# Kernel optimization log

Measured on AMD Instinct MI355X. Metric: run time of the kernel, lower is better.

The kernel has to match this reference:

```python
import jax, jax.numpy as jnp
import numpy as np


def setup_inputs() -> dict:
    key = jax.random.key(0)
    kx, ky, kw = jax.random.split(key, 3)
    B, N, M = 8, 4096, 4096
    x = jax.random.normal(kx, (B, N, 3), dtype=jnp.float32)
    y = jax.random.normal(ky, (B, M, 3), dtype=jnp.float32)
    weight = jax.random.uniform(kw, (B,), dtype=jnp.float32)
    return {"x": x, "y": y, "weight": weight}


def reference(x, y, weight):
    # (mathematically identical to sum((x-y)^2), avoids the (B,N,M,3) tensor)
    x2 = jnp.sum(x * x, axis=-1)                     # (B, N)
    y2 = jnp.sum(y * y, axis=-1)                     # (B, M)
    xy = jnp.einsum('bnd,bmd->bnm', x, y)            # (B, N, M)
    dist = jnp.maximum(x2[:, :, None] + y2[:, None, :] - 2.0 * xy, 0.0)
    dist_x_min = jnp.min(dist, axis=2)               # (B, N) nearest-in-y per x
    dist_y_min = jnp.min(dist, axis=1)               # (B, M) nearest-in-x per y
    # point_reduction='mean', bidirectional=True
    loss = jnp.mean(dist_x_min, axis=1) + jnp.mean(dist_y_min, axis=1)  # (B,)
    loss = loss * weight
    # batch_reduction='mean'
    return jnp.mean(loss)
```

## Files before the change

kernel.cpp:

```cpp
#include <hip/hip_runtime.h>
#include <math.h>


constexpr int BATCH = 8;
constexpr int NP    = 4096;
constexpr int T     = 1024;
constexpr int QPB   = 256;
constexpr int KPT   = 8;
constexpr int S     = 32;
constexpr int TPS   = 128;

__global__ __launch_bounds__(T, 4) void chamfer_main(
    const float* __restrict__ x, const float* __restrict__ y,
    const float* __restrict__ w, float* __restrict__ ps)
{
    const int bid = blockIdx.x;
    const int dir = bid >> 7;
    const int b   = (bid >> 4) & 7;
    const int qc  = bid & 15;

    const float* q = dir ? y : x;
    const float* t = dir ? x : y;

    __shared__ float4 ty[NP];
    __shared__ float  pmin[S / 2][QPB];
    __shared__ float  qn[QPB];
    __shared__ float  rsum[T / 64];

    const int tid = threadIdx.x;

    const float* tb = t + (size_t)b * NP * 3;
    for (int j = tid; j < NP; j += T) {
        float t0 = tb[3 * j + 0];
        float t1 = tb[3 * j + 1];
        float t2 = tb[3 * j + 2];
        ty[j] = make_float4(t0, t1, t2, fmaf(t0, t0, fmaf(t1, t1, t2 * t2)));
    }

    const int qrow  = tid & 31;
    const int slice = tid >> 5;
    const int n0 = b * NP + qc * QPB + qrow * KPT;
    const float4* qb = reinterpret_cast<const float4*>(q + (size_t)n0 * 3);
    float4 v0 = qb[0], v1 = qb[1], v2 = qb[2], v3 = qb[3], v4 = qb[4], v5 = qb[5];
    float px[KPT][3] = {
        {v0.x, v0.y, v0.z}, {v0.w, v1.x, v1.y},
        {v1.z, v1.w, v2.x}, {v2.y, v2.z, v2.w},
        {v3.x, v3.y, v3.z}, {v3.w, v4.x, v4.y},
        {v4.z, v4.w, v5.x}, {v5.y, v5.z, v5.w},
    };
    float xn[KPT][3], mn[KPT];
    #pragma unroll
    for (int k = 0; k < KPT; ++k) {
        float x2 = fmaf(px[k][0], px[k][0],
                   fmaf(px[k][1], px[k][1], px[k][2] * px[k][2]));
        if (slice == 0) qn[qrow * KPT + k] = x2;
        #pragma unroll
        for (int d = 0; d < 3; ++d) xn[k][d] = -2.0f * px[k][d];
        mn[k] = INFINITY;
    }

    __syncthreads();

    const int j0 = slice * TPS;
    #pragma unroll 4
    for (int j = j0; j < j0 + TPS; j += 2) {
        float4 ta = ty[j];
        float4 tc = ty[j + 1];
        #pragma unroll
        for (int k = 0; k < KPT; ++k) {
            float da = fmaf(xn[k][0], ta.x,
                       fmaf(xn[k][1], ta.y, fmaf(xn[k][2], ta.z, ta.w)));
            float db = fmaf(xn[k][0], tc.x,
                       fmaf(xn[k][1], tc.y, fmaf(xn[k][2], tc.z, tc.w)));
            float m;
            asm("v_min3_f32 %0, %1, %2, %3"
                : "=v"(m) : "v"(mn[k]), "v"(da), "v"(db));
            mn[k] = m;
        }
    }

    #pragma unroll
    for (int k = 0; k < KPT; ++k)
        mn[k] = fminf(mn[k], __shfl_xor(mn[k], 32, 64));
    if ((slice & 1) == 0) {
        #pragma unroll
        for (int k = 0; k < KPT; ++k)
            pmin[slice >> 1][qrow * KPT + k] = mn[k];
    }
    __syncthreads();

    float val = 0.0f;
    if (tid < QPB) {
        float m = pmin[0][tid];
        #pragma unroll
        for (int s = 1; s < S / 2; ++s) m = fminf(m, pmin[s][tid]);
        val = fmaxf(qn[tid] + m, 0.0f);
    }

    for (int off = 32; off; off >>= 1) val += __shfl_down(val, off, 64);
    if ((tid & 63) == 0) rsum[tid >> 6] = val;
    __syncthreads();
    if (tid == 0) {
        float s = 0.0f;
        #pragma unroll
        for (int i = 0; i < T / 64; ++i) s += rsum[i];
        ps[bid] = s * w[b] * (1.0f / ((float)NP * (float)BATCH));
    }
}

__global__ __launch_bounds__(256) void chamfer_final(
    const float* __restrict__ ps, float* __restrict__ out)
{
    const int tid = threadIdx.x;
    float v = ps[tid];
    for (int off = 32; off; off >>= 1) v += __shfl_down(v, off, 64);
    __shared__ float red[4];
    if ((tid & 63) == 0) red[tid >> 6] = v;
    __syncthreads();
    if (tid == 0) out[0] = (red[0] + red[1]) + (red[2] + red[3]);
}

extern "C" void kernel_launch(void* const* d_in, const int* in_sizes, int n_in,
                              void* d_out, int out_size, void* d_ws, size_t ws_size,
                              hipStream_t stream) {
    const float* x = (const float*)d_in[0];
    const float* y = (const float*)d_in[1];
    const float* w = (const float*)d_in[2];
    float* out = (float*)d_out;
    float* ps  = (float*)d_ws;

    chamfer_main<<<256, T, 0, stream>>>(x, y, w, ps);
    chamfer_final<<<1, 256, 0, stream>>>(ps, out);
}
```

Before: 26.91 us.

## Raise queries per thread to sixteen and shrink final reduction to one wavefront

Each thread now holds 16 query points instead of 8 and scans 64 target points instead of 128, so every shared-memory float4 load of a target is reused across twice as many queries. The cross-lane min reduction gains a second shuffle step because four slices now share a wavefront. The final reduction kernel uses a single 64-thread wavefront with float4 loads and no shared memory or barrier. The trade-off is more registers per thread under a 1024-thread launch bound, which risks spills or lower occupancy.

```diff
diff --git a/kernel.cpp b/kernel.cpp
--- a/kernel.cpp
+++ b/kernel.cpp
@@ -6,9 +6,9 @@
 constexpr int NP    = 4096;
 constexpr int T     = 1024;
 constexpr int QPB   = 256;
-constexpr int KPT   = 8;
-constexpr int S     = 32;
-constexpr int TPS   = 128;
+constexpr int KPT   = 16;
+constexpr int S     = 64;
+constexpr int TPS   = 64;
 
 __global__ __launch_bounds__(T, 4) void chamfer_main(
     const float* __restrict__ x, const float* __restrict__ y,
@@ -23,7 +23,7 @@
     const float* t = dir ? x : y;
 
     __shared__ float4 ty[NP];
-    __shared__ float  pmin[S / 2][QPB];
+    __shared__ float  pmin[S / 4][QPB];
     __shared__ float  qn[QPB];
     __shared__ float  rsum[T / 64];
 
@@ -37,32 +37,33 @@
         ty[j] = make_float4(t0, t1, t2, fmaf(t0, t0, fmaf(t1, t1, t2 * t2)));
     }
 
-    const int qrow  = tid & 31;
-    const int slice = tid >> 5;
+    const int qrow  = tid & 15;
+    const int slice = tid >> 4;
     const int n0 = b * NP + qc * QPB + qrow * KPT;
     const float4* qb = reinterpret_cast<const float4*>(q + (size_t)n0 * 3);
-    float4 v0 = qb[0], v1 = qb[1], v2 = qb[2], v3 = qb[3], v4 = qb[4], v5 = qb[5];
-    float px[KPT][3] = {
-        {v0.x, v0.y, v0.z}, {v0.w, v1.x, v1.y},
-        {v1.z, v1.w, v2.x}, {v2.y, v2.z, v2.w},
-        {v3.x, v3.y, v3.z}, {v3.w, v4.x, v4.y},
-        {v4.z, v4.w, v5.x}, {v5.y, v5.z, v5.w},
-    };
+    float qf[48];
+    #pragma unroll
+    for (int i = 0; i < 12; ++i) {
+        float4 v = qb[i];
+        qf[4 * i + 0] = v.x; qf[4 * i + 1] = v.y;
+        qf[4 * i + 2] = v.z; qf[4 * i + 3] = v.w;
+    }
     float xn[KPT][3], mn[KPT];
     #pragma unroll
     for (int k = 0; k < KPT; ++k) {
-        float x2 = fmaf(px[k][0], px[k][0],
-                   fmaf(px[k][1], px[k][1], px[k][2] * px[k][2]));
-        if (slice == 0) qn[qrow * KPT + k] = x2;
-        #pragma unroll
-        for (int d = 0; d < 3; ++d) xn[k][d] = -2.0f * px[k][d];
+        float c0 = qf[3 * k], c1 = qf[3 * k + 1], c2 = qf[3 * k + 2];
+        if (slice == 0)
+            qn[qrow * KPT + k] = fmaf(c0, c0, fmaf(c1, c1, c2 * c2));
+        xn[k][0] = -2.0f * c0;
+        xn[k][1] = -2.0f * c1;
+        xn[k][2] = -2.0f * c2;
         mn[k] = INFINITY;
     }
 
     __syncthreads();
 
     const int j0 = slice * TPS;
-    #pragma unroll 4
+    #pragma unroll 2
     for (int j = j0; j < j0 + TPS; j += 2) {
         float4 ta = ty[j];
         float4 tc = ty[j + 1];
@@ -80,12 +81,14 @@
     }
 
     #pragma unroll
-    for (int k = 0; k < KPT; ++k)
+    for (int k = 0; k < KPT; ++k) {
         mn[k] = fminf(mn[k], __shfl_xor(mn[k], 32, 64));
-    if ((slice & 1) == 0) {
+        mn[k] = fminf(mn[k], __shfl_xor(mn[k], 16, 64));
+    }
+    if ((slice & 3) == 0) {
         #pragma unroll
         for (int k = 0; k < KPT; ++k)
-            pmin[slice >> 1][qrow * KPT + k] = mn[k];
+            pmin[slice >> 2][qrow * KPT + k] = mn[k];
     }
     __syncthreads();
 
@@ -93,7 +96,7 @@
     if (tid < QPB) {
         float m = pmin[0][tid];
         #pragma unroll
-        for (int s = 1; s < S / 2; ++s) m = fminf(m, pmin[s][tid]);
+        for (int s = 1; s < S / 4; ++s) m = fminf(m, pmin[s][tid]);
         val = fmaxf(qn[tid] + m, 0.0f);
     }
 
@@ -108,16 +111,14 @@
     }
 }
 
-__global__ __launch_bounds__(256) void chamfer_final(
+__global__ __launch_bounds__(64) void chamfer_final(
     const float* __restrict__ ps, float* __restrict__ out)
 {
-    const int tid = threadIdx.x;
-    float v = ps[tid];
-    for (int off = 32; off; off >>= 1) v += __shfl_down(v, off, 64);
-    __shared__ float red[4];
-    if ((tid & 63) == 0) red[tid >> 6] = v;
-    __syncthreads();
-    if (tid == 0) out[0] = (red[0] + red[1]) + (red[2] + red[3]);
+    const int l = threadIdx.x;
+    float4 v = reinterpret_cast<const float4*>(ps)[l];
+    float s = (v.x + v.y) + (v.z + v.w);
+    for (int off = 32; off; off >>= 1) s += __shfl_down(s, off, 64);
+    if (l == 0) out[0] = s;
 }
 
 extern "C" void kernel_launch(void* const* d_in, const int* in_sizes, int n_in,
@@ -130,5 +131,5 @@
     float* ps  = (float*)d_ws;
 
     chamfer_main<<<256, T, 0, stream>>>(x, y, w, ps);
-    chamfer_final<<<1, 256, 0, stream>>>(ps, out);
+    chamfer_final<<<1, 64, 0, stream>>>(ps, out);
 }
```

Result: slower. 28.41 us (+5.6%).

## Split target reads between LDS and direct global loads, shrink final reduction

Applied to the files above, without the earlier changes.

Only the first half of the target points is staged in shared memory. Slices 16-31 read their target points straight from global memory and recompute the squared norm per point. This halves LDS usage and staging work, and relieves LDS bandwidth pressure in the inner loop, in exchange for global-load latency on half the waves. The final reduction kernel also shrinks to one wavefront using float4 loads.

```diff
diff --git a/kernel.cpp b/kernel.cpp
--- a/kernel.cpp
+++ b/kernel.cpp
@@ -9,6 +9,7 @@
 constexpr int KPT   = 8;
 constexpr int S     = 32;
 constexpr int TPS   = 128;
+constexpr int NTL   = 2048;
 
 __global__ __launch_bounds__(T, 4) void chamfer_main(
     const float* __restrict__ x, const float* __restrict__ y,
@@ -22,7 +23,7 @@
     const float* q = dir ? y : x;
     const float* t = dir ? x : y;
 
-    __shared__ float4 ty[NP];
+    __shared__ float4 ty[NTL];
     __shared__ float  pmin[S / 2][QPB];
     __shared__ float  qn[QPB];
     __shared__ float  rsum[T / 64];
@@ -30,7 +31,7 @@
     const int tid = threadIdx.x;
 
     const float* tb = t + (size_t)b * NP * 3;
-    for (int j = tid; j < NP; j += T) {
+    for (int j = tid; j < NTL; j += T) {
         float t0 = tb[3 * j + 0];
         float t1 = tb[3 * j + 1];
         float t2 = tb[3 * j + 2];
@@ -61,21 +62,43 @@
 
     __syncthreads();
 
-    const int j0 = slice * TPS;
-    #pragma unroll 4
-    for (int j = j0; j < j0 + TPS; j += 2) {
-        float4 ta = ty[j];
-        float4 tc = ty[j + 1];
-        #pragma unroll
-        for (int k = 0; k < KPT; ++k) {
-            float da = fmaf(xn[k][0], ta.x,
-                       fmaf(xn[k][1], ta.y, fmaf(xn[k][2], ta.z, ta.w)));
-            float db = fmaf(xn[k][0], tc.x,
-                       fmaf(xn[k][1], tc.y, fmaf(xn[k][2], tc.z, tc.w)));
-            float m;
-            asm("v_min3_f32 %0, %1, %2, %3"
-                : "=v"(m) : "v"(mn[k]), "v"(da), "v"(db));
-            mn[k] = m;
+    if (slice < 16) {
+        const int j0 = slice * TPS;
+        #pragma unroll 4
+        for (int j = j0; j < j0 + TPS; j += 2) {
+            float4 ta = ty[j];
+            float4 tc = ty[j + 1];
+            #pragma unroll
+            for (int k = 0; k < KPT; ++k) {
+                float da = fmaf(xn[k][0], ta.x,
+                           fmaf(xn[k][1], ta.y, fmaf(xn[k][2], ta.z, ta.w)));
+                float db = fmaf(xn[k][0], tc.x,
+                           fmaf(xn[k][1], tc.y, fmaf(xn[k][2], tc.z, tc.w)));
+                float m;
+                asm("v_min3_f32 %0, %1, %2, %3"
+                    : "=v"(m) : "v"(mn[k]), "v"(da), "v"(db));
+                mn[k] = m;
+            }
+        }
+    } else {
+        const float* gt = tb + (size_t)(slice * TPS) * 3;
+        #pragma unroll 4
+        for (int i = 0; i < TPS; i += 2) {
+            float a0 = gt[3 * i + 0], a1 = gt[3 * i + 1], a2 = gt[3 * i + 2];
+            float c0 = gt[3 * i + 3], c1 = gt[3 * i + 4], c2 = gt[3 * i + 5];
+            float aw = fmaf(a0, a0, fmaf(a1, a1, a2 * a2));
+            float cw = fmaf(c0, c0, fmaf(c1, c1, c2 * c2));
+            #pragma unroll
+            for (int k = 0; k < KPT; ++k) {
+                float da = fmaf(xn[k][0], a0,
+                           fmaf(xn[k][1], a1, fmaf(xn[k][2], a2, aw)));
+                float db = fmaf(xn[k][0], c0,
+                           fmaf(xn[k][1], c1, fmaf(xn[k][2], c2, cw)));
+                float m;
+                asm("v_min3_f32 %0, %1, %2, %3"
+                    : "=v"(m) : "v"(mn[k]), "v"(da), "v"(db));
+                mn[k] = m;
+            }
         }
     }
 
@@ -108,16 +131,14 @@
     }
 }
 
-__global__ __launch_bounds__(256) void chamfer_final(
+__global__ __launch_bounds__(64) void chamfer_final(
     const float* __restrict__ ps, float* __restrict__ out)
 {
-    const int tid = threadIdx.x;
-    float v = ps[tid];
-    for (int off = 32; off; off >>= 1) v += __shfl_down(v, off, 64);
-    __shared__ float red[4];
-    if ((tid & 63) == 0) red[tid >> 6] = v;
-    __syncthreads();
-    if (tid == 0) out[0] = (red[0] + red[1]) + (red[2] + red[3]);
+    const int l = threadIdx.x;
+    float4 v = reinterpret_cast<const float4*>(ps)[l];
+    float s = (v.x + v.y) + (v.z + v.w);
+    for (int off = 32; off; off >>= 1) s += __shfl_down(s, off, 64);
+    if (l == 0) out[0] = s;
 }
 
 extern "C" void kernel_launch(void* const* d_in, const int* in_sizes, int n_in,
@@ -130,5 +151,5 @@
     float* ps  = (float*)d_ws;
 
     chamfer_main<<<256, T, 0, stream>>>(x, y, w, ps);
-    chamfer_final<<<1, 256, 0, stream>>>(ps, out);
+    chamfer_final<<<1, 64, 0, stream>>>(ps, out);
 }
```

After: 28.82 us. 1.07x slower.
